# Optimization experiments

Hardware: AMD Instinct MI355X
Metric: run time of the kernel (lower is better)

## Reference

```python
import jax, jax.numpy as jnp
import numpy as np

N_QUBIT = 22
K = 2  # entangling layers; params has K+1 rotation layers

# CNOT as a (2,2,2,2) tensor: U[c_out, t_out, c_in, t_in]
_CNOT = np.zeros((2, 2, 2, 2), np.complex64)
_CNOT[0, 0, 0, 0] = _CNOT[0, 1, 0, 1] = _CNOT[1, 1, 1, 0] = _CNOT[1, 0, 1, 1] = 1.0
CNOT = jnp.asarray(_CNOT)


def rot_mats(p):
    """Fuse RZ(t0), RX(t1), RZ(t2) per qubit into one 2x2 unitary.
    p: (L, 3n) float -> (L, n, 2, 2) complex64. Matrix = RZ(t2) @ RX(t1) @ RZ(t0)."""
    L = p.shape[0]
    n = p.shape[1] // 3
    half = (p.reshape(L, n, 3) * 0.5)
    a, b, c = half[..., 0], half[..., 1], half[..., 2]
    e = lambda t: jnp.exp(-1j * t.astype(jnp.complex64))  # e^{-i t}
    cb = jnp.cos(b).astype(jnp.complex64)
    sb = (-1j) * jnp.sin(b).astype(jnp.complex64)
    m00 = e(a + c) * cb          # e^{-i(a+c)} cos b
    m01 = e(c - a) * sb          # -i e^{ i(a-c)} sin b
    m10 = e(a - c) * sb          # -i e^{-i(a-c)} sin b
    m11 = e(-(a + c)) * cb       # e^{ i(a+c)} cos b
    row0 = jnp.stack([m00, m01], axis=-1)
    row1 = jnp.stack([m10, m11], axis=-1)
    return jnp.stack([row0, row1], axis=-2)


def apply_1q(state, G, q):
    # contract 2x2 gate with axis q of the (2,)*n state tensor
    return jnp.moveaxis(jnp.tensordot(G, state, axes=((1,), (q,))), 0, q)


def apply_cnot(state, c, t):
    return jnp.moveaxis(jnp.tensordot(CNOT, state, axes=((2, 3), (c, t))), (0, 1), (c, t))


def setup_inputs() -> dict:
    key = jax.random.key(0)
    params = jax.random.normal(key, (K + 1, 3 * N_QUBIT), dtype=jnp.float32) * np.float32(np.pi)
    return {"params": params}


def reference(params) -> jnp.ndarray:
    n = params.shape[1] // 3
    k = params.shape[0] - 1
    G = rot_mats(params)  # (k+1, n, 2, 2)
    state = jnp.zeros((2,) * n, dtype=jnp.complex64).at[(0,) * n].set(1.0)
    for layer in range(k):
        for q in range(n):
            state = apply_1q(state, G[layer, q], q)
        for q in range(n):  # ring entangler (pairs=None branch)
            state = apply_cnot(state, q, (q + 1) % n)
    for q in range(n):  # final rotation layer
        state = apply_1q(state, G[k, q], q)
    return (state.real ** 2 + state.imag ** 2).reshape(-1)  # probs over 2^n basis states
```

## Files before the change

kernel.cpp:

```cpp
#include <hip/hip_runtime.h>


typedef float2 cplx;

__device__ __forceinline__ cplx cmul(cplx a, cplx b) {
    return make_float2(fmaf(a.x, b.x, -a.y * b.y), fmaf(a.x, b.y, a.y * b.x));
}

#define T_COL1 0
#define T_G1   64
#define T_G2   192
#define T_A0   320
#define T_BT   576

template<int BIT>
__device__ __forceinline__ void gate32(cplx* a, const cplx* __restrict__ g) {
    const cplx g00 = g[0], g01 = g[1], g10 = g[2], g11 = g[3];
#pragma unroll
    for (int p = 0; p < 16; ++p) {
        int i0 = ((p >> BIT) << (BIT + 1)) | (p & ((1 << BIT) - 1));
        int i1 = i0 | (1 << BIT);
        cplx A = a[i0], B = a[i1];
        float ax = fmaf(g00.x, A.x, fmaf(-g00.y, A.y, fmaf(g01.x, B.x, -g01.y * B.y)));
        float ay = fmaf(g00.x, A.y, fmaf( g00.y, A.x, fmaf(g01.x, B.y,  g01.y * B.x)));
        float bx = fmaf(g10.x, A.x, fmaf(-g10.y, A.y, fmaf(g11.x, B.x, -g11.y * B.y)));
        float by = fmaf(g10.x, A.y, fmaf( g10.y, A.x, fmaf(g11.x, B.y,  g11.y * B.x)));
        a[i0] = make_float2(ax, ay);
        a[i1] = make_float2(bx, by);
    }
}

template<int BIT>
__device__ __forceinline__ void gate32f(cplx* a, const cplx* __restrict__ g, int s) {
    const bool flip = (s >> BIT) & 1;
    cplx g00 = g[0], g01 = g[1], g10 = g[2], g11 = g[3];
    if (flip) {
        cplx t = g00; g00 = g11; g11 = t;
        t = g01; g01 = g10; g10 = t;
    }
#pragma unroll
    for (int p = 0; p < 16; ++p) {
        int i0 = ((p >> BIT) << (BIT + 1)) | (p & ((1 << BIT) - 1));
        int i1 = i0 | (1 << BIT);
        cplx A = a[i0], B = a[i1];
        float ax = fmaf(g00.x, A.x, fmaf(-g00.y, A.y, fmaf(g01.x, B.x, -g01.y * B.y)));
        float ay = fmaf(g00.x, A.y, fmaf( g00.y, A.x, fmaf(g01.x, B.y,  g01.y * B.x)));
        float bx = fmaf(g10.x, A.x, fmaf(-g10.y, A.y, fmaf(g11.x, B.x, -g11.y * B.y)));
        float by = fmaf(g10.x, A.y, fmaf( g10.y, A.x, fmaf(g11.x, B.y,  g11.y * B.x)));
        a[i0] = make_float2(ax, ay);
        a[i1] = make_float2(bx, by);
    }
}

__device__ constexpr int relab(int m) {
    int g = m ^ (m >> 1);
    int m0 = m & 1;
    return (g & 0x07F7) | (((g >> 3) & 1) << 3)
         | ((((g >> 11) & 1) ^ m0) << 11) | ((((m >> 12) & 1) ^ m0) << 12);
}
__device__ constexpr int mjof(int j) { return (j & 15) | (((j >> 4) & 1) << 5); }

__global__ __launch_bounds__(256) void k_setup(const float* __restrict__ p, cplx* __restrict__ tab) {
    int tid = threadIdx.x;
    if (tid < 22) {
        int j = tid, q = 21 - j;
        {
            float a = 0.5f * p[3 * q], b = 0.5f * p[3 * q + 1], c = 0.5f * p[3 * q + 2];
            float cb = cosf(b), sb = sinf(b);
            tab[T_COL1 + 2 * j + 0] = make_float2(cosf(a + c) * cb, -sinf(a + c) * cb);
            float ex = cosf(a - c), ey = -sinf(a - c);
            tab[T_COL1 + 2 * j + 1] = make_float2(ey * sb, -ex * sb);
        }
        for (int L = 1; L <= 2; ++L) {
            const float* pp = p + 66 * L;
            float a = 0.5f * pp[3 * q], b = 0.5f * pp[3 * q + 1], c = 0.5f * pp[3 * q + 2];
            float cb = cosf(b), sb = sinf(b);
            cplx eac  = make_float2(cosf(a + c), -sinf(a + c));
            cplx eca  = make_float2(cosf(c - a), -sinf(c - a));
            cplx eacp = make_float2(eac.x, -eac.y);
            cplx ecap = make_float2(eca.x, -eca.y);
            cplx* G = tab + (L == 1 ? T_G1 : T_G2) + 4 * j;
            G[0] = make_float2(eac.x * cb, eac.y * cb);
            G[1] = make_float2(eca.y * sb, -eca.x * sb);
            G[2] = make_float2(ecap.y * sb, -ecap.x * sb);
            G[3] = make_float2(eacp.x * cb, eacp.y * cb);
        }
    }
    __syncthreads();
    {
        int i = tid;
        cplx v = make_float2(1.f, 0.f);
        for (int jj = 0; jj <= 6; ++jj) {
            int xb = ((i >> jj) ^ (i >> (jj + 1))) & 1;
            v = cmul(v, tab[T_COL1 + 2 * jj + xb]);
        }
        tab[T_A0 + i] = v;
    }
    if (tid < 128) {
        int i = tid;
        cplx v = make_float2(1.f, 0.f);
        for (int j = 7; j <= 11; ++j) {
            int xb = ((i >> (j - 7)) ^ (i >> (j - 6))) & 1;
            v = cmul(v, tab[T_COL1 + 2 * j + xb]);
        }
        int xb12 = ((i >> 5) ^ (i >> 6)) & 1;
        v = cmul(v, tab[T_COL1 + 24 + xb12]);
        tab[T_BT + i] = v;
    }
}

__global__ __launch_bounds__(256) void kA(const cplx* __restrict__ tab, cplx* __restrict__ bufA) {
    __shared__ cplx tile[8192];
    const int wg = blockIdx.x;
    const int tid = threadIdx.x;
    const cplx* col1 = tab + T_COL1;
    const cplx* G1 = tab + T_G1;
    const int v13 = wg & 1, v20 = (wg >> 7) & 1, v21 = (wg >> 8) & 1;
    cplx H = make_float2(1.f, 0.f);
#pragma unroll
    for (int j = 13; j <= 19; ++j) {
        int xb = ((wg >> (j - 13)) ^ (wg >> (j - 12))) & 1;
        H = cmul(H, col1[2 * j + xb]);
    }
    {
        int l0 = tid & 1;
        cplx s2 = cmul(col1[40 + (l0 ^ v20 ^ v21)], col1[42 + (l0 ^ v21)]);
        H = cmul(cmul(H, s2), tab[T_A0 + tid]);
    }
    cplx a[32];
#pragma unroll
    for (int j = 0; j < 32; ++j)
        a[j] = cmul(H, tab[T_BT + ((j << 1) | (tid >> 7) | (v13 << 6))]);
    gate32<0>(a, G1 + 4 * 8);  gate32<1>(a, G1 + 4 * 9);  gate32<2>(a, G1 + 4 * 10);
    gate32<3>(a, G1 + 4 * 11); gate32<4>(a, G1 + 4 * 12);
#pragma unroll
    for (int j = 0; j < 32; ++j) tile[tid + (j << 8)] = a[j];
    __syncthreads();
    {
        const int b1 = (tid & 7) | ((tid >> 3) << 8);
#pragma unroll
        for (int j = 0; j < 32; ++j) a[j] = tile[b1 + (j << 3)];
        gate32<0>(a, G1 + 4 * 3); gate32<1>(a, G1 + 4 * 4); gate32<2>(a, G1 + 4 * 5);
        gate32<3>(a, G1 + 4 * 6); gate32<4>(a, G1 + 4 * 7);
        __syncthreads();
#pragma unroll
        for (int j = 0; j < 32; ++j) tile[b1 + (j << 3)] = a[j];
    }
    __syncthreads();
    {
        char* tb = (char*)tile;
        const int b2 = tid << 8;
        const int x2 = (tid & 31) << 3;
#pragma unroll
        for (int j = 0; j < 32; ++j) a[j] = *(cplx*)(tb + (b2 | ((j << 3) ^ x2)));
        gate32f<0>(a, G1 + 4 * 0, tid); gate32f<1>(a, G1 + 4 * 1, tid);
        gate32f<2>(a, G1 + 4 * 2, tid);
        __syncthreads();
#pragma unroll
        for (int j = 0; j < 32; ++j) *(cplx*)(tb + (b2 | ((j << 3) ^ x2))) = a[j];
    }
    __syncthreads();
    {
        const char* tb = (const char*)tile;
        float4* gA = (float4*)(bufA + (wg << 13) + 2 * tid);
#pragma unroll
        for (int j = 0; j < 16; ++j)
            gA[j << 8] = *(const float4*)(tb + 16 * tid + (j << 12));
    }
}

__global__ __launch_bounds__(256) void kB(const cplx* __restrict__ tab,
                                          const cplx* __restrict__ bufA, cplx* __restrict__ bufB) {
    __shared__ cplx tile[8192];
    const int wg = blockIdx.x;
    const int tid = threadIdx.x;
    const cplx* G1 = tab + T_G1;
    const cplx* G2 = tab + T_G2;
    const int F = __popc(wg) & 1;
    int W = (wg >> 8) << 8;
#pragma unroll
    for (int t = 0; t < 8; ++t) W |= (__popc(wg >> t) & 1) << t;
    cplx a[32];
    {
        const cplx* gA = bufA + ((tid & 15) | (wg << 4) | ((tid >> 4) << 18));
#pragma unroll
        for (int j = 0; j < 32; ++j) a[j] = gA[j << 13];
    }
    gate32<0>(a, G1 + 4 * 13); gate32<1>(a, G1 + 4 * 14); gate32<2>(a, G1 + 4 * 15);
    gate32<3>(a, G1 + 4 * 16); gate32<4>(a, G1 + 4 * 17);
    {
        const int b0 = (tid & 15) | ((tid >> 4) << 9);
#pragma unroll
        for (int j = 0; j < 32; ++j) tile[b0 + (j << 4)] = a[j];
    }
    __syncthreads();
    {
        const int b1 = (tid & 15) | (((tid >> 4) & 15) << 5);
#pragma unroll
        for (int j = 0; j < 32; ++j)
            a[j] = tile[b1 + ((j & 15) << 9) + (((j >> 4) & 1) << 4)];
        gate32<0>(a, G1 + 4 * 18); gate32<1>(a, G1 + 4 * 19);
        gate32<2>(a, G1 + 4 * 20); gate32<3>(a, G1 + 4 * 21);
        __syncthreads();
#pragma unroll
        for (int j = 0; j < 32; ++j)
            tile[b1 + ((j & 15) << 9) + (((j >> 4) & 1) << 4)] = a[j];
    }
    __syncthreads();
    {
        char* tb = (char*)tile;
        const int s = (tid >> 1) & 15;
        const int mt = s | ((tid & 1) << 4) | ((tid >> 1) << 6);
        const int Bt  = (relab(mt) ^ (F << 3)) << 3;
        const int Bt2 = mt << 3;
#pragma unroll
        for (int j = 0; j < 32; ++j)
            a[j] = *(cplx*)(tb + (Bt ^ (relab(mjof(j)) << 3)));
        gate32f<0>(a, G2 + 4 * 0, s); gate32f<1>(a, G2 + 4 * 1, s);
        gate32f<2>(a, G2 + 4 * 2, s); gate32f<3>(a, G2 + 4 * 3, s);
        gate32<4>(a, G2 + 4 * 14);
        __syncthreads();
#pragma unroll
        for (int j = 0; j < 32; ++j)
            *(cplx*)(tb + (Bt2 ^ (mjof(j) << 3))) = a[j];
    }
    __syncthreads();
    {
        const int b3 = (tid & 15) | (((tid >> 4) & 1) << 4) | (((tid >> 5) & 1) << 5)
                     | (((tid >> 6) & 1) << 11) | (((tid >> 7) & 1) << 12);
#pragma unroll
        for (int j = 0; j < 32; ++j) a[j] = tile[b3 + (j << 6)];
        gate32<0>(a, G2 + 4 * 15); gate32<1>(a, G2 + 4 * 16); gate32<2>(a, G2 + 4 * 17);
        gate32<3>(a, G2 + 4 * 18); gate32<4>(a, G2 + 4 * 19);
        __syncthreads();
#pragma unroll
        for (int j = 0; j < 32; ++j) tile[b3 + (j << 6)] = a[j];
    }
    __syncthreads();
    {
#pragma unroll
        for (int j = 0; j < 32; ++j) a[j] = tile[tid + (j << 8)];
        gate32<3>(a, G2 + 4 * 20); gate32<4>(a, G2 + 4 * 21);
        const int Y9 = W ^ (((tid >> 4) & 1) ? 0x1FF : 0);
        cplx* gB = bufB + ((tid & 15) | (Y9 << 4) | (((tid >> 4) & 15) << 13));
#pragma unroll
        for (int j = 0; j < 32; ++j) gB[j << 17] = a[j];
    }
}

__global__ __launch_bounds__(512) void kC(const cplx* __restrict__ tab,
                                          const cplx* __restrict__ bufB, float* __restrict__ out) {
    extern __shared__ cplx tileC[];
    const int wg = blockIdx.x;
    const int tid = threadIdx.x;
    const cplx* G2 = tab + T_G2;
    const int base = wg << 14;
    cplx a[32];
    {
        const cplx* gB = bufB + base + ((tid & 15) | ((tid >> 4) << 9));
#pragma unroll
        for (int j = 0; j < 32; ++j) a[j] = gB[j << 4];
    }
    gate32<0>(a, G2 + 4 * 4); gate32<1>(a, G2 + 4 * 5); gate32<2>(a, G2 + 4 * 6);
    gate32<3>(a, G2 + 4 * 7); gate32<4>(a, G2 + 4 * 8);
    {
        const int b0 = (tid & 15) | ((tid >> 4) << 9);
#pragma unroll
        for (int j = 0; j < 32; ++j) tileC[b0 + (j << 4)] = a[j];
    }
    __syncthreads();
#pragma unroll
    for (int j = 0; j < 32; ++j) a[j] = tileC[tid + (j << 9)];
    gate32<0>(a, G2 + 4 * 9);  gate32<1>(a, G2 + 4 * 10); gate32<2>(a, G2 + 4 * 11);
    gate32<3>(a, G2 + 4 * 12); gate32<4>(a, G2 + 4 * 13);
    {
        float* gout = out + base + tid;
#pragma unroll
        for (int j = 0; j < 32; ++j)
            gout[j << 9] = fmaf(a[j].x, a[j].x, a[j].y * a[j].y);
    }
}

extern "C" void kernel_launch(void* const* d_in, const int* in_sizes, int n_in,
                              void* d_out, int out_size, void* d_ws, size_t ws_size,
                              hipStream_t stream) {
    const float* params = (const float*)d_in[0];
    cplx* bufA = (cplx*)d_ws;
    cplx* bufB = bufA + (1 << 22);
    cplx* tab  = bufA + (1 << 23);
    float* out = (float*)d_out;

    k_setup<<<1, 256, 0, stream>>>(params, tab);
    kA<<<512, 256, 0, stream>>>(tab, bufA);
    kB<<<512, 256, 0, stream>>>(tab, bufA, bufB);
    kC<<<256, 512, 131072, stream>>>(tab, bufB, out);
}
```

Baseline: 121.6 us.

## Halve per-thread amplitudes to 16 and double threads per block in all kernels

```diff
diff --git a/kernel.cpp b/kernel.cpp
--- a/kernel.cpp
+++ b/kernel.cpp
@@ -13,11 +13,11 @@
 #define T_A0   320
 #define T_BT   576
 
-template<int BIT>
-__device__ __forceinline__ void gate32(cplx* a, const cplx* __restrict__ g) {
+template<int BIT, int N>
+__device__ __forceinline__ void gateN(cplx* a, const cplx* __restrict__ g) {
     const cplx g00 = g[0], g01 = g[1], g10 = g[2], g11 = g[3];
 #pragma unroll
-    for (int p = 0; p < 16; ++p) {
+    for (int p = 0; p < N / 2; ++p) {
         int i0 = ((p >> BIT) << (BIT + 1)) | (p & ((1 << BIT) - 1));
         int i1 = i0 | (1 << BIT);
         cplx A = a[i0], B = a[i1];
@@ -30,8 +30,8 @@
     }
 }
 
-template<int BIT>
-__device__ __forceinline__ void gate32f(cplx* a, const cplx* __restrict__ g, int s) {
+template<int BIT, int N>
+__device__ __forceinline__ void gateNf(cplx* a, const cplx* __restrict__ g, int s) {
     const bool flip = (s >> BIT) & 1;
     cplx g00 = g[0], g01 = g[1], g10 = g[2], g11 = g[3];
     if (flip) {
@@ -39,7 +39,7 @@
         t = g01; g01 = g10; g10 = t;
     }
 #pragma unroll
-    for (int p = 0; p < 16; ++p) {
+    for (int p = 0; p < N / 2; ++p) {
         int i0 = ((p >> BIT) << (BIT + 1)) | (p & ((1 << BIT) - 1));
         int i1 = i0 | (1 << BIT);
         cplx A = a[i0], B = a[i1];
@@ -58,7 +58,9 @@
     return (g & 0x07F7) | (((g >> 3) & 1) << 3)
          | ((((g >> 11) & 1) ^ m0) << 11) | ((((m >> 12) & 1) ^ m0) << 12);
 }
-__device__ constexpr int mjof(int j) { return (j & 15) | (((j >> 4) & 1) << 5); }
+__device__ constexpr int relab4(int x) {
+    return (x ^ (x >> 1)) | ((x & 1) ? 0x1800 : 0);
+}
 
 __global__ __launch_bounds__(256) void k_setup(const float* __restrict__ p, cplx* __restrict__ tab) {
     int tid = threadIdx.x;
@@ -109,7 +111,7 @@
     }
 }
 
-__global__ __launch_bounds__(256) void kA(const cplx* __restrict__ tab, cplx* __restrict__ bufA) {
+__global__ __launch_bounds__(512, 4) void kA(const cplx* __restrict__ tab, cplx* __restrict__ bufA) {
     __shared__ cplx tile[8192];
     const int wg = blockIdx.x;
     const int tid = threadIdx.x;
@@ -125,52 +127,58 @@
     {
         int l0 = tid & 1;
         cplx s2 = cmul(col1[40 + (l0 ^ v20 ^ v21)], col1[42 + (l0 ^ v21)]);
-        H = cmul(cmul(H, s2), tab[T_A0 + tid]);
-    }
-    cplx a[32];
-#pragma unroll
-    for (int j = 0; j < 32; ++j)
-        a[j] = cmul(H, tab[T_BT + ((j << 1) | (tid >> 7) | (v13 << 6))]);
-    gate32<0>(a, G1 + 4 * 8);  gate32<1>(a, G1 + 4 * 9);  gate32<2>(a, G1 + 4 * 10);
-    gate32<3>(a, G1 + 4 * 11); gate32<4>(a, G1 + 4 * 12);
-#pragma unroll
-    for (int j = 0; j < 32; ++j) tile[tid + (j << 8)] = a[j];
-    __syncthreads();
-    {
-        const int b1 = (tid & 7) | ((tid >> 3) << 8);
-#pragma unroll
-        for (int j = 0; j < 32; ++j) a[j] = tile[b1 + (j << 3)];
-        gate32<0>(a, G1 + 4 * 3); gate32<1>(a, G1 + 4 * 4); gate32<2>(a, G1 + 4 * 5);
-        gate32<3>(a, G1 + 4 * 6); gate32<4>(a, G1 + 4 * 7);
-        __syncthreads();
-#pragma unroll
-        for (int j = 0; j < 32; ++j) tile[b1 + (j << 3)] = a[j];
-    }
-    __syncthreads();
-    {
-        char* tb = (char*)tile;
-        const int b2 = tid << 8;
-        const int x2 = (tid & 31) << 3;
-#pragma unroll
-        for (int j = 0; j < 32; ++j) a[j] = *(cplx*)(tb + (b2 | ((j << 3) ^ x2)));
-        gate32f<0>(a, G1 + 4 * 0, tid); gate32f<1>(a, G1 + 4 * 1, tid);
-        gate32f<2>(a, G1 + 4 * 2, tid);
-        __syncthreads();
-#pragma unroll
-        for (int j = 0; j < 32; ++j) *(cplx*)(tb + (b2 | ((j << 3) ^ x2))) = a[j];
+        H = cmul(cmul(H, s2), tab[T_A0 + (tid & 255)]);
+    }
+    cplx a[16];
+#pragma unroll
+    for (int j = 0; j < 16; ++j)
+        a[j] = cmul(H, tab[T_BT + (((tid >> 7) & 3) | (j << 2) | (v13 << 6))]);
+    gateN<0,16>(a, G1 + 4 * 9);  gateN<1,16>(a, G1 + 4 * 10);
+    gateN<2,16>(a, G1 + 4 * 11); gateN<3,16>(a, G1 + 4 * 12);
+#pragma unroll
+    for (int j = 0; j < 16; ++j) tile[tid + (j << 9)] = a[j];
+    __syncthreads();
+    {
+        const int b1 = (tid & 31) | ((tid >> 5) << 9);
+#pragma unroll
+        for (int j = 0; j < 16; ++j) a[j] = tile[b1 + (j << 5)];
+        gateN<0,16>(a, G1 + 4 * 5); gateN<1,16>(a, G1 + 4 * 6);
+        gateN<2,16>(a, G1 + 4 * 7); gateN<3,16>(a, G1 + 4 * 8);
+        __syncthreads();
+#pragma unroll
+        for (int j = 0; j < 16; ++j) tile[b1 + (j << 5)] = a[j];
+    }
+    __syncthreads();
+    {
+        const int s = (tid >> 1) & 15;
+        const int b2 = (tid & 1) | ((tid >> 1) << 5);
+#pragma unroll
+        for (int j = 0; j < 16; ++j) a[j] = tile[b2 + (((j ^ s) & 15) << 1)];
+        gateNf<0,16>(a, G1 + 4 * 1, s); gateNf<1,16>(a, G1 + 4 * 2, s);
+        gateNf<2,16>(a, G1 + 4 * 3, s); gateNf<3,16>(a, G1 + 4 * 4, s);
+        __syncthreads();
+#pragma unroll
+        for (int j = 0; j < 16; ++j) tile[b2 + (((j ^ s) & 15) << 1)] = a[j];
     }
     __syncthreads();
     {
         const char* tb = (const char*)tile;
-        float4* gA = (float4*)(bufA + (wg << 13) + 2 * tid);
-#pragma unroll
-        for (int j = 0; j < 16; ++j)
-            gA[j << 8] = *(const float4*)(tb + 16 * tid + (j << 12));
-    }
-}
-
-__global__ __launch_bounds__(256) void kB(const cplx* __restrict__ tab,
-                                          const cplx* __restrict__ bufA, cplx* __restrict__ bufB) {
+#pragma unroll
+        for (int h = 0; h < 8; ++h) {
+            float4 f = *(const float4*)(tb + 16 * tid + (h << 13));
+            a[2 * h]     = make_float2(f.x, f.y);
+            a[2 * h + 1] = make_float2(f.z, f.w);
+        }
+        gateN<0,16>(a, G1 + 4 * 0);
+        float4* gA = (float4*)(bufA + (wg << 13));
+#pragma unroll
+        for (int h = 0; h < 8; ++h)
+            gA[tid | (h << 9)] = make_float4(a[2*h].x, a[2*h].y, a[2*h+1].x, a[2*h+1].y);
+    }
+}
+
+__global__ __launch_bounds__(512, 4) void kB(const cplx* __restrict__ tab,
+                                             const cplx* __restrict__ bufA, cplx* __restrict__ bufB) {
     __shared__ cplx tile[8192];
     const int wg = blockIdx.x;
     const int tid = threadIdx.x;
@@ -180,104 +188,112 @@
     int W = (wg >> 8) << 8;
 #pragma unroll
     for (int t = 0; t < 8; ++t) W |= (__popc(wg >> t) & 1) << t;
-    cplx a[32];
-    {
-        const cplx* gA = bufA + ((tid & 15) | (wg << 4) | ((tid >> 4) << 18));
-#pragma unroll
-        for (int j = 0; j < 32; ++j) a[j] = gA[j << 13];
-    }
-    gate32<0>(a, G1 + 4 * 13); gate32<1>(a, G1 + 4 * 14); gate32<2>(a, G1 + 4 * 15);
-    gate32<3>(a, G1 + 4 * 16); gate32<4>(a, G1 + 4 * 17);
-    {
-        const int b0 = (tid & 15) | ((tid >> 4) << 9);
-#pragma unroll
-        for (int j = 0; j < 32; ++j) tile[b0 + (j << 4)] = a[j];
-    }
-    __syncthreads();
-    {
-        const int b1 = (tid & 15) | (((tid >> 4) & 15) << 5);
-#pragma unroll
-        for (int j = 0; j < 32; ++j)
-            a[j] = tile[b1 + ((j & 15) << 9) + (((j >> 4) & 1) << 4)];
-        gate32<0>(a, G1 + 4 * 18); gate32<1>(a, G1 + 4 * 19);
-        gate32<2>(a, G1 + 4 * 20); gate32<3>(a, G1 + 4 * 21);
-        __syncthreads();
-#pragma unroll
-        for (int j = 0; j < 32; ++j)
-            tile[b1 + ((j & 15) << 9) + (((j >> 4) & 1) << 4)] = a[j];
-    }
-    __syncthreads();
-    {
-        char* tb = (char*)tile;
+    cplx a[16];
+    {
+        const cplx* gA = bufA + ((tid & 15) | (wg << 4) | (((tid >> 4) & 31) << 17));
+#pragma unroll
+        for (int j = 0; j < 16; ++j) a[j] = gA[j << 13];
+        gateN<0,16>(a, G1 + 4 * 13); gateN<1,16>(a, G1 + 4 * 14);
+        gateN<2,16>(a, G1 + 4 * 15); gateN<3,16>(a, G1 + 4 * 16);
+        const int b0 = (tid & 15) | ((tid >> 4) << 8);
+#pragma unroll
+        for (int j = 0; j < 16; ++j) tile[b0 + (j << 4)] = a[j];
+    }
+    __syncthreads();
+    {
+        const int b1 = (tid & 255) | ((tid >> 8) << 12);
+#pragma unroll
+        for (int j = 0; j < 16; ++j) a[j] = tile[b1 + (j << 8)];
+        gateN<0,16>(a, G1 + 4 * 17); gateN<1,16>(a, G1 + 4 * 18);
+        gateN<2,16>(a, G1 + 4 * 19); gateN<3,16>(a, G1 + 4 * 20);
+        __syncthreads();
+#pragma unroll
+        for (int j = 0; j < 16; ++j) tile[b1 + (j << 8)] = a[j];
+    }
+    __syncthreads();
+    {
+#pragma unroll
+        for (int j = 0; j < 16; ++j) a[j] = tile[tid + (j << 9)];
+        gateN<3,16>(a, G1 + 4 * 21);
+        __syncthreads();
+#pragma unroll
+        for (int j = 0; j < 16; ++j) tile[tid + (j << 9)] = a[j];
+    }
+    __syncthreads();
+    {
         const int s = (tid >> 1) & 15;
-        const int mt = s | ((tid & 1) << 4) | ((tid >> 1) << 6);
-        const int Bt  = (relab(mt) ^ (F << 3)) << 3;
-        const int Bt2 = mt << 3;
-#pragma unroll
-        for (int j = 0; j < 32; ++j)
-            a[j] = *(cplx*)(tb + (Bt ^ (relab(mjof(j)) << 3)));
-        gate32f<0>(a, G2 + 4 * 0, s); gate32f<1>(a, G2 + 4 * 1, s);
-        gate32f<2>(a, G2 + 4 * 2, s); gate32f<3>(a, G2 + 4 * 3, s);
-        gate32<4>(a, G2 + 4 * 14);
-        __syncthreads();
-#pragma unroll
-        for (int j = 0; j < 32; ++j)
-            *(cplx*)(tb + (Bt2 ^ (mjof(j) << 3))) = a[j];
-    }
-    __syncthreads();
-    {
-        const int b3 = (tid & 15) | (((tid >> 4) & 1) << 4) | (((tid >> 5) & 1) << 5)
-                     | (((tid >> 6) & 1) << 11) | (((tid >> 7) & 1) << 12);
-#pragma unroll
-        for (int j = 0; j < 32; ++j) a[j] = tile[b3 + (j << 6)];
-        gate32<0>(a, G2 + 4 * 15); gate32<1>(a, G2 + 4 * 16); gate32<2>(a, G2 + 4 * 17);
-        gate32<3>(a, G2 + 4 * 18); gate32<4>(a, G2 + 4 * 19);
-        __syncthreads();
-#pragma unroll
-        for (int j = 0; j < 32; ++j) tile[b3 + (j << 6)] = a[j];
-    }
-    __syncthreads();
-    {
-#pragma unroll
-        for (int j = 0; j < 32; ++j) a[j] = tile[tid + (j << 8)];
-        gate32<3>(a, G2 + 4 * 20); gate32<4>(a, G2 + 4 * 21);
+        const int Bte = relab(tid << 4) ^ (F << 3) ^ relab4(s);
+        const int Bw  = (tid << 4) | s;
+#pragma unroll
+        for (int j = 0; j < 16; ++j) a[j] = tile[Bte ^ relab4(j)];
+        gateNf<0,16>(a, G2 + 4 * 0, s); gateNf<1,16>(a, G2 + 4 * 1, s);
+        gateNf<2,16>(a, G2 + 4 * 2, s); gateNf<3,16>(a, G2 + 4 * 3, s);
+        __syncthreads();
+#pragma unroll
+        for (int j = 0; j < 16; ++j) tile[Bw ^ j] = a[j];
+    }
+    __syncthreads();
+    {
+        const int b4 = (tid & 31) | ((tid >> 5) << 9);
+#pragma unroll
+        for (int j = 0; j < 16; ++j) a[j] = tile[b4 + (j << 5)];
+        gateN<0,16>(a, G2 + 4 * 14); gateN<1,16>(a, G2 + 4 * 15);
+        gateN<2,16>(a, G2 + 4 * 16); gateN<3,16>(a, G2 + 4 * 17);
+        __syncthreads();
+#pragma unroll
+        for (int j = 0; j < 16; ++j) tile[b4 + (j << 5)] = a[j];
+    }
+    __syncthreads();
+    {
+#pragma unroll
+        for (int j = 0; j < 16; ++j) a[j] = tile[tid + (j << 9)];
+        gateN<0,16>(a, G2 + 4 * 18); gateN<1,16>(a, G2 + 4 * 19);
+        gateN<2,16>(a, G2 + 4 * 20); gateN<3,16>(a, G2 + 4 * 21);
         const int Y9 = W ^ (((tid >> 4) & 1) ? 0x1FF : 0);
-        cplx* gB = bufB + ((tid & 15) | (Y9 << 4) | (((tid >> 4) & 15) << 13));
-#pragma unroll
-        for (int j = 0; j < 32; ++j) gB[j << 17] = a[j];
-    }
-}
-
-__global__ __launch_bounds__(512) void kC(const cplx* __restrict__ tab,
-                                          const cplx* __restrict__ bufB, float* __restrict__ out) {
+        cplx* gB = bufB + ((tid & 15) | (Y9 << 4) | (((tid >> 4) & 31) << 13));
+#pragma unroll
+        for (int j = 0; j < 16; ++j) gB[j << 18] = a[j];
+    }
+}
+
+__global__ __launch_bounds__(1024, 4) void kC(const cplx* __restrict__ tab,
+                                              const cplx* __restrict__ bufB, float* __restrict__ out) {
     extern __shared__ cplx tileC[];
     const int wg = blockIdx.x;
     const int tid = threadIdx.x;
     const cplx* G2 = tab + T_G2;
     const int base = wg << 14;
-    cplx a[32];
-    {
-        const cplx* gB = bufB + base + ((tid & 15) | ((tid >> 4) << 9));
-#pragma unroll
-        for (int j = 0; j < 32; ++j) a[j] = gB[j << 4];
-    }
-    gate32<0>(a, G2 + 4 * 4); gate32<1>(a, G2 + 4 * 5); gate32<2>(a, G2 + 4 * 6);
-    gate32<3>(a, G2 + 4 * 7); gate32<4>(a, G2 + 4 * 8);
-    {
-        const int b0 = (tid & 15) | ((tid >> 4) << 9);
-#pragma unroll
-        for (int j = 0; j < 32; ++j) tileC[b0 + (j << 4)] = a[j];
-    }
-    __syncthreads();
-#pragma unroll
-    for (int j = 0; j < 32; ++j) a[j] = tileC[tid + (j << 9)];
-    gate32<0>(a, G2 + 4 * 9);  gate32<1>(a, G2 + 4 * 10); gate32<2>(a, G2 + 4 * 11);
-    gate32<3>(a, G2 + 4 * 12); gate32<4>(a, G2 + 4 * 13);
-    {
+    cplx a[16];
+    {
+        const cplx* gB = bufB + base + ((tid & 15) | ((tid >> 4) << 8));
+#pragma unroll
+        for (int j = 0; j < 16; ++j) a[j] = gB[j << 4];
+        gateN<0,16>(a, G2 + 4 * 4); gateN<1,16>(a, G2 + 4 * 5);
+        gateN<2,16>(a, G2 + 4 * 6); gateN<3,16>(a, G2 + 4 * 7);
+        const int b0 = (tid & 15) | ((tid >> 4) << 8);
+#pragma unroll
+        for (int j = 0; j < 16; ++j) tileC[b0 + (j << 4)] = a[j];
+    }
+    __syncthreads();
+    {
+        const int b1 = (tid & 255) | ((tid >> 8) << 12);
+#pragma unroll
+        for (int j = 0; j < 16; ++j) a[j] = tileC[b1 + (j << 8)];
+        gateN<0,16>(a, G2 + 4 * 8);  gateN<1,16>(a, G2 + 4 * 9);
+        gateN<2,16>(a, G2 + 4 * 10); gateN<3,16>(a, G2 + 4 * 11);
+        __syncthreads();
+#pragma unroll
+        for (int j = 0; j < 16; ++j) tileC[b1 + (j << 8)] = a[j];
+    }
+    __syncthreads();
+    {
+#pragma unroll
+        for (int j = 0; j < 16; ++j) a[j] = tileC[tid + (j << 10)];
+        gateN<2,16>(a, G2 + 4 * 12); gateN<3,16>(a, G2 + 4 * 13);
         float* gout = out + base + tid;
 #pragma unroll
-        for (int j = 0; j < 32; ++j)
-            gout[j << 9] = fmaf(a[j].x, a[j].x, a[j].y * a[j].y);
+        for (int j = 0; j < 16; ++j)
+            gout[j << 10] = fmaf(a[j].x, a[j].x, a[j].y * a[j].y);
     }
 }
 
@@ -291,7 +307,7 @@
     float* out = (float*)d_out;
 
     k_setup<<<1, 256, 0, stream>>>(params, tab);
-    kA<<<512, 256, 0, stream>>>(tab, bufA);
-    kB<<<512, 256, 0, stream>>>(tab, bufA, bufB);
-    kC<<<256, 512, 131072, stream>>>(tab, bufB, out);
-}
+    kA<<<512, 512, 0, stream>>>(tab, bufA);
+    kB<<<512, 512, 0, stream>>>(tab, bufA, bufB);
+    kC<<<256, 1024, 131072, stream>>>(tab, bufB, out);
+}
```

New measurement: 115.4 us. -5.1%, faster.
